# Kernel tuning notes

Measured on AMD Instinct MI355X. Metric: run time of the kernel, lower is better.

The kernel has to match this reference:

```python
import jax, jax.numpy as jnp
import numpy as np

B, NQ, NKV, D = 2, 2048, 2048, 1024
N_HEADS = 16
D_H = D // N_HEADS


def setup_inputs() -> dict:
    key = jax.random.key(0)
    ks = jax.random.split(key, 10)
    s = 0.02  # weight init scale
    return {
        "q": jax.random.normal(ks[0], (B, NQ, D), jnp.float32),
        "kv": jax.random.normal(ks[1], (B, NKV, D), jnp.float32),
        "Wq": jax.random.normal(ks[2], (D, D), jnp.float32) * s,
        "bq": jnp.zeros((D,), jnp.float32),
        "Wk": jax.random.normal(ks[3], (D, D), jnp.float32) * s,
        "bk": jnp.zeros((D,), jnp.float32),
        "Wv": jax.random.normal(ks[4], (D, D), jnp.float32) * s,
        "bv": jnp.zeros((D,), jnp.float32),
        "Wo": jax.random.normal(ks[5], (D, D), jnp.float32) * s,
        "bo": jnp.zeros((D,), jnp.float32),
    }


def reference(q, kv, Wq, bq, Wk, bk, Wv, bv, Wo, bo):
    # Linear projections (torch Linear: x @ W.T + b)
    qh = q @ Wq.T + bq   # [B, NQ, D]
    kh = kv @ Wk.T + bk  # [B, NKV, D]
    vh = kv @ Wv.T + bv  # [B, NKV, D]
    # Split heads: [B, N, H, d_h]
    qh = qh.reshape(B, NQ, N_HEADS, D_H)
    kh = kh.reshape(B, NKV, N_HEADS, D_H)
    vh = vh.reshape(B, NKV, N_HEADS, D_H)
    scale = 1.0 / jnp.sqrt(jnp.asarray(D_H, qh.dtype))
    # QK^T per head: [B, H, NQ, NKV]
    scores = jnp.einsum("bqhd,bkhd->bhqk", qh, kh) * scale
    att = jax.nn.softmax(scores, axis=-1)
    # dropout p=0.0 -> identity
    out = jnp.einsum("bhqk,bkhd->bqhd", att, vh)  # [B, NQ, H, d_h]
    out = out.reshape(B, NQ, D)
    return out @ Wo.T + bo
```

## Files before the change

kernel.cpp:

```cpp
#include <hip/hip_runtime.h>
#include <cstddef>
#include <cstdint>

using half4v  = __attribute__((ext_vector_type(4))) _Float16;
using half8   = __attribute__((ext_vector_type(8))) _Float16;
using floatx4 = __attribute__((ext_vector_type(4))) float;

#define B_   2
#define NQ_  2048
#define DM   1024
#define NH_  16
#define DH_  64
#define NTILES 32

__device__ __forceinline__ void async16(const _Float16* g, _Float16* l) {
    __builtin_amdgcn_global_load_lds(
        (const __attribute__((address_space(1))) unsigned int*)g,
        (__attribute__((address_space(3))) unsigned int*)l, 16, 0, 0);
}

__global__ __launch_bounds__(256) void cvt_all(
        const float* __restrict__ q,  const float* __restrict__ kv,
        const float* __restrict__ wq, const float* __restrict__ wk,
        const float* __restrict__ wv, const float* __restrict__ wo,
        _Float16* __restrict__ dq,  _Float16* __restrict__ dkv,
        _Float16* __restrict__ dwq, _Float16* __restrict__ dwk,
        _Float16* __restrict__ dwv, _Float16* __restrict__ dwo) {
    int blk = blockIdx.x;
    const float* s;
    _Float16* d;
    int base;
    if (blk < 2048)      { s = q;  d = dq;  base = blk; }
    else if (blk < 4096) { s = kv; d = dkv; base = blk - 2048; }
    else if (blk < 4608) { s = wq; d = dwq; base = blk - 4096; }
    else if (blk < 5120) { s = wk; d = dwk; base = blk - 4608; }
    else if (blk < 5632) { s = wv; d = dwv; base = blk - 5120; }
    else                 { s = wo; d = dwo; base = blk - 5632; }
    int i = base * 256 + threadIdx.x;
    const float4* s4 = (const float4*)s;
    float4 a = s4[2 * i], b = s4[2 * i + 1];
    half8 h;
    h[0] = (_Float16)a.x; h[1] = (_Float16)a.y; h[2] = (_Float16)a.z; h[3] = (_Float16)a.w;
    h[4] = (_Float16)b.x; h[5] = (_Float16)b.y; h[6] = (_Float16)b.z; h[7] = (_Float16)b.w;
    ((half8*)d)[i] = h;
}

__global__ __launch_bounds__(256, 3) void proj_qkv(
        const _Float16* __restrict__ q16, const _Float16* __restrict__ kv16,
        const _Float16* __restrict__ wqp, const _Float16* __restrict__ wkp,
        const _Float16* __restrict__ wvp,
        const float* __restrict__ bqp, const float* __restrict__ bkp,
        const float* __restrict__ bvp,
        _Float16* __restrict__ qh, _Float16* __restrict__ kh,
        _Float16* __restrict__ vt) {
    __shared__ _Float16 As[128 * 64];
    __shared__ _Float16 Bs[128 * 64];

    const int which = blockIdx.x >> 8;
    const int sub = blockIdx.x & 255;
    const _Float16* A = (which == 0) ? q16 : kv16;
    const _Float16* W = (which == 0) ? wqp : (which == 1) ? wkp : wvp;
    const float* bias = (which == 0) ? bqp : (which == 1) ? bkp : bvp;

    const int t = threadIdx.x;
    const int w = t >> 6, lane = t & 63;
    const int r16 = lane & 15, quad = lane >> 4;
    const int bn = sub & 7, bm = sub >> 3;
    const int m0 = bm * 128, n0 = bn * 128;
    const int wm = w >> 1, wn = w & 1;

    floatx4 acc[4][4];
#pragma unroll
    for (int i = 0; i < 4; i++)
#pragma unroll
        for (int j = 0; j < 4; j++)
#pragma unroll
            for (int r = 0; r < 4; r++) acc[i][j][r] = 0.f;

    const int ph0 = quad ^ (r16 & 7), ph1 = ph0 ^ 4;

    for (int k0 = 0; k0 < DM; k0 += 64) {
        __syncthreads();
#pragma unroll
        for (int i = 0; i < 4; i++) {
            int P = i * 256 + t;
            int m = P >> 3, c = (P & 7) ^ (m & 7);
            async16(A + (size_t)(m0 + m) * DM + k0 + c * 8, &As[P * 8]);
            async16(W + (size_t)(n0 + m) * DM + k0 + c * 8, &Bs[P * 8]);
        }
        asm volatile("s_waitcnt vmcnt(0)" ::: "memory");
        __syncthreads();

        half8 af[4][2], bf[4][2];
#pragma unroll
        for (int mi = 0; mi < 4; mi++) {
            int m = wm * 64 + mi * 16 + r16;
            af[mi][0] = ((const half8*)As)[m * 8 + ph0];
            af[mi][1] = ((const half8*)As)[m * 8 + ph1];
        }
#pragma unroll
        for (int ni = 0; ni < 4; ni++) {
            int n = wn * 64 + ni * 16 + r16;
            bf[ni][0] = ((const half8*)Bs)[n * 8 + ph0];
            bf[ni][1] = ((const half8*)Bs)[n * 8 + ph1];
        }
#pragma unroll
        for (int kd = 0; kd < 2; kd++)
#pragma unroll
            for (int mi = 0; mi < 4; mi++)
#pragma unroll
                for (int ni = 0; ni < 4; ni++)
                    acc[mi][ni] = __builtin_amdgcn_mfma_f32_16x16x32_f16(
                        af[mi][kd], bf[ni][kd], acc[mi][ni], 0, 0, 0);
    }

    if (which < 2) {
        _Float16* C = (which == 0) ? qh : kh;
        const float esc = (which == 0) ? 0.125f : 1.0f;
#pragma unroll
        for (int mi = 0; mi < 4; mi++)
#pragma unroll
            for (int r = 0; r < 4; r++) {
                int row = m0 + wm * 64 + mi * 16 + quad * 4 + r;
#pragma unroll
                for (int ni = 0; ni < 4; ni++) {
                    int col = n0 + wn * 64 + ni * 16 + r16;
                    C[(size_t)row * DM + col] = (_Float16)((acc[mi][ni][r] + bias[col]) * esc);
                }
            }
    } else {
#pragma unroll
        for (int mi = 0; mi < 4; mi++) {
            int krow = m0 + wm * 64 + mi * 16 + quad * 4;
            int bb = krow >> 11, kk = krow & 2047;
#pragma unroll
            for (int ni = 0; ni < 4; ni++) {
                int col = n0 + wn * 64 + ni * 16 + r16;
                int hh = col >> 6, dd = col & 63;
                float bv = bias[col];
                half4v pk;
#pragma unroll
                for (int r = 0; r < 4; r++) pk[r] = (_Float16)(acc[mi][ni][r] + bv);
                *(half4v*)&vt[((size_t)((bb * NH_ + hh) * DH_ + dd)) * NQ_ + kk] = pk;
            }
        }
    }
}

__global__ __launch_bounds__(256, 2) void attn_mfma(const _Float16* __restrict__ Qg,
                                                    const _Float16* __restrict__ Kg,
                                                    const _Float16* __restrict__ Vt,
                                                    _Float16* __restrict__ Og) {
    __shared__ _Float16 Ps[128 * 64];
    __shared__ _Float16 Ks[2][64 * 64];
    __shared__ _Float16 Vs[2][64 * 64];

    const int t = threadIdx.x, w = t >> 6, lane = t & 63;
    const int r16 = lane & 15, quad = lane >> 4;
    const int qt = blockIdx.x & 15;
    const int bh = blockIdx.x >> 4;
    const int b = bh >> 4, h = bh & 15;

    const _Float16* qbase = Qg + (size_t)(b * NQ_ + qt * 128) * DM + h * DH_;
    const _Float16* kbase = Kg + (size_t)(b * NQ_) * DM + h * DH_;
    const _Float16* vbase = Vt + (size_t)bh * DH_ * NQ_;

#pragma unroll
    for (int i = 0; i < 4; i++) {
        int P = i * 256 + t;
        int m = P >> 3, c = (P & 7) ^ (m & 7);
        async16(qbase + (size_t)m * DM + c * 8, &Ps[P * 8]);
    }
#pragma unroll
    for (int i = 0; i < 2; i++) {
        int P = i * 256 + t;
        int m = P >> 3, c = (P & 7) ^ (m & 7);
        async16(kbase + (size_t)m * DM + c * 8, &Ks[0][P * 8]);
        async16(vbase + (size_t)m * NQ_ + c * 8, &Vs[0][P * 8]);
    }
    asm volatile("s_waitcnt vmcnt(0)" ::: "memory");
    __syncthreads();

    const int ph0 = quad ^ (r16 & 7), ph1 = ph0 ^ 4;
    half8 Qf[2][2];
#pragma unroll
    for (int mi = 0; mi < 2; mi++) {
        int m = w * 32 + mi * 16 + r16;
        Qf[mi][0] = ((const half8*)Ps)[m * 8 + ph0];
        Qf[mi][1] = ((const half8*)Ps)[m * 8 + ph1];
    }

    floatx4 oaccT[2][4];
    float lacc[2] = {0.f, 0.f};
#pragma unroll
    for (int mi = 0; mi < 2; mi++)
#pragma unroll
        for (int nd = 0; nd < 4; nd++)
#pragma unroll
            for (int r = 0; r < 4; r++) oaccT[mi][nd][r] = 0.f;

    for (int kt = 0; kt < NTILES; kt++) {
        const int cur = kt & 1;
        asm volatile("s_waitcnt vmcnt(0)" ::: "memory");
        __syncthreads();

        if (kt + 1 < NTILES) {
            const int nxt = cur ^ 1;
#pragma unroll
            for (int i = 0; i < 2; i++) {
                int P = i * 256 + t;
                int m = P >> 3, c = (P & 7) ^ (m & 7);
                async16(kbase + (size_t)((kt + 1) * 64 + m) * DM + c * 8, &Ks[nxt][P * 8]);
                async16(vbase + (size_t)m * NQ_ + (kt + 1) * 64 + c * 8, &Vs[nxt][P * 8]);
            }
        }

        floatx4 sacc[2][4];
#pragma unroll
        for (int mi = 0; mi < 2; mi++)
#pragma unroll
            for (int nk = 0; nk < 4; nk++)
#pragma unroll
                for (int r = 0; r < 4; r++) sacc[mi][nk][r] = 0.f;
#pragma unroll
        for (int kd = 0; kd < 2; kd++)
#pragma unroll
            for (int nk = 0; nk < 4; nk++) {
                half8 kf = ((const half8*)Ks[cur])[(nk * 16 + r16) * 8 + (kd ? ph1 : ph0)];
                sacc[0][nk] = __builtin_amdgcn_mfma_f32_16x16x32_f16(kf, Qf[0][kd], sacc[0][nk], 0, 0, 0);
                sacc[1][nk] = __builtin_amdgcn_mfma_f32_16x16x32_f16(kf, Qf[1][kd], sacc[1][nk], 0, 0, 0);
            }

#pragma unroll
        for (int mi = 0; mi < 2; mi++) {
            int q = w * 32 + mi * 16 + r16;
#pragma unroll
            for (int nk = 0; nk < 4; nk++) {
                float p0 = __expf(sacc[mi][nk][0]);
                float p1 = __expf(sacc[mi][nk][1]);
                float p2 = __expf(sacc[mi][nk][2]);
                float p3 = __expf(sacc[mi][nk][3]);
                lacc[mi] += (p0 + p1) + (p2 + p3);
                half4v pk;
                pk[0] = (_Float16)p0; pk[1] = (_Float16)p1;
                pk[2] = (_Float16)p2; pk[3] = (_Float16)p3;
                int phys = (nk * 2 + (quad >> 1)) ^ (r16 & 7);
                *(half4v*)&Ps[q * 64 + phys * 8 + (quad & 1) * 4] = pk;
            }
        }

#pragma unroll
        for (int ks = 0; ks < 2; ks++) {
            half8 pf[2];
#pragma unroll
            for (int mi = 0; mi < 2; mi++) {
                int q = w * 32 + mi * 16 + r16;
                pf[mi] = ((const half8*)Ps)[q * 8 + ((ks * 4 + quad) ^ (r16 & 7))];
            }
#pragma unroll
            for (int nd = 0; nd < 4; nd++) {
                half8 vf = ((const half8*)Vs[cur])[(nd * 16 + r16) * 8 + ((ks * 4 + quad) ^ (r16 & 7))];
                oaccT[0][nd] = __builtin_amdgcn_mfma_f32_16x16x32_f16(vf, pf[0], oaccT[0][nd], 0, 0, 0);
                oaccT[1][nd] = __builtin_amdgcn_mfma_f32_16x16x32_f16(vf, pf[1], oaccT[1][nd], 0, 0, 0);
            }
        }
    }

#pragma unroll
    for (int mi = 0; mi < 2; mi++) {
        float l = lacc[mi];
        l += __shfl_xor(l, 16);
        l += __shfl_xor(l, 32);
        float inv = 1.f / l;
        int qrow = b * NQ_ + qt * 128 + w * 32 + mi * 16 + r16;
#pragma unroll
        for (int nd = 0; nd < 4; nd++) {
            half4v o;
#pragma unroll
            for (int r = 0; r < 4; r++) o[r] = (_Float16)(oaccT[mi][nd][r] * inv);
            *(half4v*)&Og[(size_t)qrow * DM + h * DH_ + nd * 16 + quad * 4] = o;
        }
    }
}

__global__ __launch_bounds__(256, 2) void gemm_o(const _Float16* __restrict__ A,
                                                 const _Float16* __restrict__ W,
                                                 const float* __restrict__ bias,
                                                 float* __restrict__ C) {
    __shared__ _Float16 As[128 * 64];
    __shared__ _Float16 Bs[64 * 64];

    const int t = threadIdx.x;
    const int w = t >> 6, lane = t & 63;
    const int r16 = lane & 15, quad = lane >> 4;
    const int bn = blockIdx.x & 15, bm = blockIdx.x >> 4;
    const int m0 = bm * 128, n0 = bn * 64;
    const int wm = w >> 1, wn = w & 1;

    floatx4 acc[4][2];
#pragma unroll
    for (int i = 0; i < 4; i++)
#pragma unroll
        for (int j = 0; j < 2; j++)
#pragma unroll
            for (int r = 0; r < 4; r++) acc[i][j][r] = 0.f;

    const int ph0 = quad ^ (r16 & 7), ph1 = ph0 ^ 4;

    for (int k0 = 0; k0 < DM; k0 += 64) {
        __syncthreads();
#pragma unroll
        for (int i = 0; i < 4; i++) {
            int P = i * 256 + t;
            int m = P >> 3, c = (P & 7) ^ (m & 7);
            async16(A + (size_t)(m0 + m) * DM + k0 + c * 8, &As[P * 8]);
        }
#pragma unroll
        for (int i = 0; i < 2; i++) {
            int P = i * 256 + t;
            int m = P >> 3, c = (P & 7) ^ (m & 7);
            async16(W + (size_t)(n0 + m) * DM + k0 + c * 8, &Bs[P * 8]);
        }
        asm volatile("s_waitcnt vmcnt(0)" ::: "memory");
        __syncthreads();

        half8 af[4][2], bf[2][2];
#pragma unroll
        for (int mi = 0; mi < 4; mi++) {
            int m = wm * 64 + mi * 16 + r16;
            af[mi][0] = ((const half8*)As)[m * 8 + ph0];
            af[mi][1] = ((const half8*)As)[m * 8 + ph1];
        }
#pragma unroll
        for (int ni = 0; ni < 2; ni++) {
            int n = wn * 32 + ni * 16 + r16;
            bf[ni][0] = ((const half8*)Bs)[n * 8 + ph0];
            bf[ni][1] = ((const half8*)Bs)[n * 8 + ph1];
        }
#pragma unroll
        for (int kd = 0; kd < 2; kd++)
#pragma unroll
            for (int mi = 0; mi < 4; mi++)
#pragma unroll
                for (int ni = 0; ni < 2; ni++)
                    acc[mi][ni] = __builtin_amdgcn_mfma_f32_16x16x32_f16(
                        af[mi][kd], bf[ni][kd], acc[mi][ni], 0, 0, 0);
    }

#pragma unroll
    for (int mi = 0; mi < 4; mi++)
#pragma unroll
        for (int r = 0; r < 4; r++) {
            int row = m0 + wm * 64 + mi * 16 + quad * 4 + r;
#pragma unroll
            for (int ni = 0; ni < 2; ni++) {
                int col = n0 + wn * 32 + ni * 16 + r16;
                C[(size_t)row * DM + col] = acc[mi][ni][r] + bias[col];
            }
        }
}

extern "C" void kernel_launch(void* const* d_in, const int* in_sizes, int n_in,
                              void* d_out, int out_size, void* d_ws, size_t ws_size,
                              hipStream_t stream) {
    const float* q  = (const float*)d_in[0];
    const float* kv = (const float*)d_in[1];
    const float* Wq = (const float*)d_in[2];
    const float* bq = (const float*)d_in[3];
    const float* Wk = (const float*)d_in[4];
    const float* bk = (const float*)d_in[5];
    const float* Wv = (const float*)d_in[6];
    const float* bv = (const float*)d_in[7];
    const float* Wo = (const float*)d_in[8];
    const float* bo = (const float*)d_in[9];

    char* ws = (char*)d_ws;
    _Float16* q16  = (_Float16*)(ws);
    _Float16* kv16 = (_Float16*)(ws + (size_t)(8  << 20));
    _Float16* w16q = (_Float16*)(ws + (size_t)(16 << 20));
    _Float16* w16k = (_Float16*)(ws + (size_t)(18 << 20));
    _Float16* w16v = (_Float16*)(ws + (size_t)(20 << 20));
    _Float16* w16o = (_Float16*)(ws + (size_t)(22 << 20));
    _Float16* qh16 = (_Float16*)(ws + (size_t)(24 << 20));
    _Float16* kh16 = (_Float16*)(ws + (size_t)(32 << 20));
    _Float16* vt16 = (_Float16*)(ws + (size_t)(40 << 20));
    _Float16* ao16 = (_Float16*)(ws + (size_t)(48 << 20));

    cvt_all<<<6144, 256, 0, stream>>>(q, kv, Wq, Wk, Wv, Wo,
                                      q16, kv16, w16q, w16k, w16v, w16o);

    proj_qkv<<<768, 256, 0, stream>>>(q16, kv16, w16q, w16k, w16v,
                                      bq, bk, bv, qh16, kh16, vt16);

    attn_mfma<<<512, 256, 0, stream>>>(qh16, kh16, vt16, ao16);

    gemm_o<<<512, 256, 0, stream>>>(ao16, w16o, bo, (float*)d_out);
}
```

Before: 215.2 us.

## Double-buffer projection GEMMs, remap blocks for locality, load V directly to registers

Both projection GEMMs (QKV and output) now double-buffer their LDS tiles, so the next K-tile is fetched while the current one is multiplied. The occupancy hints change to 2 blocks per CU for QKV and 3 for the output GEMM. Block indices in the GEMMs and in attention are remapped so that neighbouring blocks share data tiles, aiming at better L2 reuse. In attention, V is no longer staged through LDS; each lane reads its fragments straight from global memory. This saves LDS and barriers but exposes V load latency, and it could hurt if those uncoalesced strided reads are not hidden.

```diff
diff --git a/kernel.cpp b/kernel.cpp
--- a/kernel.cpp
+++ b/kernel.cpp
@@ -45,7 +45,7 @@
     ((half8*)d)[i] = h;
 }
 
-__global__ __launch_bounds__(256, 3) void proj_qkv(
+__global__ __launch_bounds__(256, 2) void proj_qkv(
         const _Float16* __restrict__ q16, const _Float16* __restrict__ kv16,
         const _Float16* __restrict__ wqp, const _Float16* __restrict__ wkp,
         const _Float16* __restrict__ wvp,
@@ -53,8 +53,8 @@
         const float* __restrict__ bvp,
         _Float16* __restrict__ qh, _Float16* __restrict__ kh,
         _Float16* __restrict__ vt) {
-    __shared__ _Float16 As[128 * 64];
-    __shared__ _Float16 Bs[128 * 64];
+    __shared__ _Float16 As[2][128 * 64];
+    __shared__ _Float16 Bs[2][128 * 64];
 
     const int which = blockIdx.x >> 8;
     const int sub = blockIdx.x & 255;
@@ -65,7 +65,8 @@
     const int t = threadIdx.x;
     const int w = t >> 6, lane = t & 63;
     const int r16 = lane & 15, quad = lane >> 4;
-    const int bn = sub & 7, bm = sub >> 3;
+    const int bm = (sub & 7) * 4 + ((sub >> 3) & 3);
+    const int bn = sub >> 5;
     const int m0 = bm * 128, n0 = bn * 128;
     const int wm = w >> 1, wn = w & 1;
 
@@ -79,30 +80,43 @@
 
     const int ph0 = quad ^ (r16 & 7), ph1 = ph0 ^ 4;
 
-    for (int k0 = 0; k0 < DM; k0 += 64) {
-        __syncthreads();
-#pragma unroll
-        for (int i = 0; i < 4; i++) {
-            int P = i * 256 + t;
-            int m = P >> 3, c = (P & 7) ^ (m & 7);
-            async16(A + (size_t)(m0 + m) * DM + k0 + c * 8, &As[P * 8]);
-            async16(W + (size_t)(n0 + m) * DM + k0 + c * 8, &Bs[P * 8]);
-        }
+#pragma unroll
+    for (int i = 0; i < 4; i++) {
+        int P = i * 256 + t;
+        int m = P >> 3, c = (P & 7) ^ (m & 7);
+        async16(A + (size_t)(m0 + m) * DM + c * 8, &As[0][P * 8]);
+        async16(W + (size_t)(n0 + m) * DM + c * 8, &Bs[0][P * 8]);
+    }
+
+    for (int kt = 0; kt < 16; kt++) {
+        const int cur = kt & 1;
         asm volatile("s_waitcnt vmcnt(0)" ::: "memory");
         __syncthreads();
 
+        if (kt + 1 < 16) {
+            const int nxt = cur ^ 1;
+            const int k0 = (kt + 1) * 64;
+#pragma unroll
+            for (int i = 0; i < 4; i++) {
+                int P = i * 256 + t;
+                int m = P >> 3, c = (P & 7) ^ (m & 7);
+                async16(A + (size_t)(m0 + m) * DM + k0 + c * 8, &As[nxt][P * 8]);
+                async16(W + (size_t)(n0 + m) * DM + k0 + c * 8, &Bs[nxt][P * 8]);
+            }
+        }
+
         half8 af[4][2], bf[4][2];
 #pragma unroll
         for (int mi = 0; mi < 4; mi++) {
             int m = wm * 64 + mi * 16 + r16;
-            af[mi][0] = ((const half8*)As)[m * 8 + ph0];
-            af[mi][1] = ((const half8*)As)[m * 8 + ph1];
+            af[mi][0] = ((const half8*)As[cur])[m * 8 + ph0];
+            af[mi][1] = ((const half8*)As[cur])[m * 8 + ph1];
         }
 #pragma unroll
         for (int ni = 0; ni < 4; ni++) {
             int n = wn * 64 + ni * 16 + r16;
-            bf[ni][0] = ((const half8*)Bs)[n * 8 + ph0];
-            bf[ni][1] = ((const half8*)Bs)[n * 8 + ph1];
+            bf[ni][0] = ((const half8*)Bs[cur])[n * 8 + ph0];
+            bf[ni][1] = ((const half8*)Bs[cur])[n * 8 + ph1];
         }
 #pragma unroll
         for (int kd = 0; kd < 2; kd++)
@@ -153,12 +167,12 @@
                                                     _Float16* __restrict__ Og) {
     __shared__ _Float16 Ps[128 * 64];
     __shared__ _Float16 Ks[2][64 * 64];
-    __shared__ _Float16 Vs[2][64 * 64];
 
     const int t = threadIdx.x, w = t >> 6, lane = t & 63;
     const int r16 = lane & 15, quad = lane >> 4;
-    const int qt = blockIdx.x & 15;
-    const int bh = blockIdx.x >> 4;
+    const int blk = blockIdx.x;
+    const int bh = (blk & 7) * 4 + ((blk >> 3) & 3);
+    const int qt = blk >> 5;
     const int b = bh >> 4, h = bh & 15;
 
     const _Float16* qbase = Qg + (size_t)(b * NQ_ + qt * 128) * DM + h * DH_;
@@ -176,7 +190,6 @@
         int P = i * 256 + t;
         int m = P >> 3, c = (P & 7) ^ (m & 7);
         async16(kbase + (size_t)m * DM + c * 8, &Ks[0][P * 8]);
-        async16(vbase + (size_t)m * NQ_ + c * 8, &Vs[0][P * 8]);
     }
     asm volatile("s_waitcnt vmcnt(0)" ::: "memory");
     __syncthreads();
@@ -211,9 +224,16 @@
                 int P = i * 256 + t;
                 int m = P >> 3, c = (P & 7) ^ (m & 7);
                 async16(kbase + (size_t)((kt + 1) * 64 + m) * DM + c * 8, &Ks[nxt][P * 8]);
-                async16(vbase + (size_t)m * NQ_ + (kt + 1) * 64 + c * 8, &Vs[nxt][P * 8]);
-            }
-        }
+            }
+        }
+
+        half8 vf[4][2];
+#pragma unroll
+        for (int nd = 0; nd < 4; nd++)
+#pragma unroll
+            for (int ks = 0; ks < 2; ks++)
+                vf[nd][ks] = *(const half8*)&vbase[(size_t)(nd * 16 + r16) * NQ_ +
+                                                   kt * 64 + ks * 32 + quad * 8];
 
         floatx4 sacc[2][4];
 #pragma unroll
@@ -259,9 +279,8 @@
             }
 #pragma unroll
             for (int nd = 0; nd < 4; nd++) {
-                half8 vf = ((const half8*)Vs[cur])[(nd * 16 + r16) * 8 + ((ks * 4 + quad) ^ (r16 & 7))];
-                oaccT[0][nd] = __builtin_amdgcn_mfma_f32_16x16x32_f16(vf, pf[0], oaccT[0][nd], 0, 0, 0);
-                oaccT[1][nd] = __builtin_amdgcn_mfma_f32_16x16x32_f16(vf, pf[1], oaccT[1][nd], 0, 0, 0);
+                oaccT[0][nd] = __builtin_amdgcn_mfma_f32_16x16x32_f16(vf[nd][ks], pf[0], oaccT[0][nd], 0, 0, 0);
+                oaccT[1][nd] = __builtin_amdgcn_mfma_f32_16x16x32_f16(vf[nd][ks], pf[1], oaccT[1][nd], 0, 0, 0);
             }
         }
     }
@@ -283,17 +302,19 @@
     }
 }
 
-__global__ __launch_bounds__(256, 2) void gemm_o(const _Float16* __restrict__ A,
+__global__ __launch_bounds__(256, 3) void gemm_o(const _Float16* __restrict__ A,
                                                  const _Float16* __restrict__ W,
                                                  const float* __restrict__ bias,
                                                  float* __restrict__ C) {
-    __shared__ _Float16 As[128 * 64];
-    __shared__ _Float16 Bs[64 * 64];
+    __shared__ _Float16 As[2][128 * 64];
+    __shared__ _Float16 Bs[2][64 * 64];
 
     const int t = threadIdx.x;
     const int w = t >> 6, lane = t & 63;
     const int r16 = lane & 15, quad = lane >> 4;
-    const int bn = blockIdx.x & 15, bm = blockIdx.x >> 4;
+    const int blk = blockIdx.x;
+    const int bm = (blk & 7) * 4 + ((blk >> 3) & 3);
+    const int bn = blk >> 5;
     const int m0 = bm * 128, n0 = bn * 64;
     const int wm = w >> 1, wn = w & 1;
 
@@ -307,35 +328,53 @@
 
     const int ph0 = quad ^ (r16 & 7), ph1 = ph0 ^ 4;
 
-    for (int k0 = 0; k0 < DM; k0 += 64) {
-        __syncthreads();
-#pragma unroll
-        for (int i = 0; i < 4; i++) {
-            int P = i * 256 + t;
-            int m = P >> 3, c = (P & 7) ^ (m & 7);
-            async16(A + (size_t)(m0 + m) * DM + k0 + c * 8, &As[P * 8]);
-        }
-#pragma unroll
-        for (int i = 0; i < 2; i++) {
-            int P = i * 256 + t;
-            int m = P >> 3, c = (P & 7) ^ (m & 7);
-            async16(W + (size_t)(n0 + m) * DM + k0 + c * 8, &Bs[P * 8]);
-        }
+#pragma unroll
+    for (int i = 0; i < 4; i++) {
+        int P = i * 256 + t;
+        int m = P >> 3, c = (P & 7) ^ (m & 7);
+        async16(A + (size_t)(m0 + m) * DM + c * 8, &As[0][P * 8]);
+    }
+#pragma unroll
+    for (int i = 0; i < 2; i++) {
+        int P = i * 256 + t;
+        int m = P >> 3, c = (P & 7) ^ (m & 7);
+        async16(W + (size_t)(n0 + m) * DM + c * 8, &Bs[0][P * 8]);
+    }
+
+    for (int kt = 0; kt < 16; kt++) {
+        const int cur = kt & 1;
         asm volatile("s_waitcnt vmcnt(0)" ::: "memory");
         __syncthreads();
 
+        if (kt + 1 < 16) {
+            const int nxt = cur ^ 1;
+            const int k0 = (kt + 1) * 64;
+#pragma unroll
+            for (int i = 0; i < 4; i++) {
+                int P = i * 256 + t;
+                int m = P >> 3, c = (P & 7) ^ (m & 7);
+                async16(A + (size_t)(m0 + m) * DM + k0 + c * 8, &As[nxt][P * 8]);
+            }
+#pragma unroll
+            for (int i = 0; i < 2; i++) {
+                int P = i * 256 + t;
+                int m = P >> 3, c = (P & 7) ^ (m & 7);
+                async16(W + (size_t)(n0 + m) * DM + k0 + c * 8, &Bs[nxt][P * 8]);
+            }
+        }
+
         half8 af[4][2], bf[2][2];
 #pragma unroll
         for (int mi = 0; mi < 4; mi++) {
             int m = wm * 64 + mi * 16 + r16;
-            af[mi][0] = ((const half8*)As)[m * 8 + ph0];
-            af[mi][1] = ((const half8*)As)[m * 8 + ph1];
+            af[mi][0] = ((const half8*)As[cur])[m * 8 + ph0];
+            af[mi][1] = ((const half8*)As[cur])[m * 8 + ph1];
         }
 #pragma unroll
         for (int ni = 0; ni < 2; ni++) {
             int n = wn * 32 + ni * 16 + r16;
-            bf[ni][0] = ((const half8*)Bs)[n * 8 + ph0];
-            bf[ni][1] = ((const half8*)Bs)[n * 8 + ph1];
+            bf[ni][0] = ((const half8*)Bs[cur])[n * 8 + ph0];
+            bf[ni][1] = ((const half8*)Bs[cur])[n * 8 + ph1];
         }
 #pragma unroll
         for (int kd = 0; kd < 2; kd++)
```

Measured after the change: 248.6 us. 1.16x slower.
